# Performance work log

Measured on AMD Instinct MI355X. Metric: run time of the kernel, lower is better.

Reference implementation:

```python
import jax, jax.numpy as jnp
import numpy as np
import math

EMBED = 1024
HEADS = 16
DHEAD = 64
B, S = 2, 2048


def setup_inputs() -> dict:
    key = jax.random.key(0)
    k1, k2, k3, k4 = jax.random.split(key, 4)
    qs = jax.random.normal(k1, (B, S, EMBED), dtype=jnp.float32)
    # causal mask, broadcast over batch (mask==0 positions are masked out)
    mask = jnp.broadcast_to(jnp.tril(jnp.ones((S, S), dtype=jnp.int32)), (B, S, S))
    # torch Linear(embed, 3*H*D, bias=False): y = x @ W^T; store transposed [E, 3HD]
    Wqkv = jax.random.normal(k2, (EMBED, 3 * HEADS * DHEAD), dtype=jnp.float32) / math.sqrt(EMBED)
    Wout = jax.random.normal(k3, (HEADS * DHEAD, EMBED), dtype=jnp.float32) / math.sqrt(HEADS * DHEAD)
    bout = jax.random.normal(k4, (EMBED,), dtype=jnp.float32) * 0.01
    return {"qs": qs, "mask": mask, "Wqkv": Wqkv, "Wout": Wout, "bout": bout}


def reference(qs, mask, Wqkv, Wout, bout):
    b, s, _ = qs.shape
    # fused QKV projection -> (B, S, 3H, D), split into q/k/v chunks of H heads
    qkv = (qs @ Wqkv).reshape(b, s, 3 * HEADS, DHEAD)
    q, k, v = qkv[:, :, :HEADS], qkv[:, :, HEADS:2 * HEADS], qkv[:, :, 2 * HEADS:]
    # scores: (B, H, Sq, Sk)
    scores = jnp.einsum("bqhd,bkhd->bhqk", q, k) / math.sqrt(DHEAD)
    scores = jnp.where(mask[:, None, :, :] == 0, jnp.float32(-1e9), scores)
    attn = jax.nn.softmax(scores, axis=-1)
    out = jnp.einsum("bhqk,bkhd->bqhd", attn, v).reshape(b, s, HEADS * DHEAD)
    return out @ Wout + bout
```

## Files before the change

kernel.cpp:

```cpp
#include <hip/hip_runtime.h>
#include <hip/hip_bf16.h>
#include <stdint.h>


typedef __attribute__((ext_vector_type(8))) short  short8;
typedef __attribute__((ext_vector_type(4))) short  short4v;
typedef __attribute__((ext_vector_type(4))) float  float4v;

#define SOFTMAX_BIAS 17.3123405f
#define QSCALE 0.18033688f

__device__ __forceinline__ unsigned short f2bf(float f) {
  unsigned int u = __builtin_bit_cast(unsigned int, f);
  u += 0x7fffu + ((u >> 16) & 1u);
  return (unsigned short)(u >> 16);
}
__device__ __forceinline__ unsigned short f2bf_trunc(float f) {
  return (unsigned short)(__builtin_bit_cast(unsigned int, f) >> 16);
}
__device__ __forceinline__ float bf2f(unsigned short s) {
  unsigned int u = ((unsigned int)s) << 16;
  return __builtin_bit_cast(float, u);
}

__device__ __forceinline__ void async_copy16(const void* g, void* l) {
  __builtin_amdgcn_global_load_lds(
      (__attribute__((address_space(1))) unsigned int*)g,
      (__attribute__((address_space(3))) unsigned int*)l, 16, 0, 0);
}

__global__ void prep_kernel(const float* __restrict__ qs,
                            const float* __restrict__ Wqkv,
                            const float* __restrict__ Wout,
                            unsigned short* __restrict__ qs_bf,
                            unsigned short* __restrict__ WqkvT,
                            unsigned short* __restrict__ WoutT) {
  __shared__ float tbuf[32][33];
  const int blk = blockIdx.x, tid = threadIdx.x;
  if (blk < 4096) {
    int i = (blk * 256 + tid) * 4;
    float4v v = *(const float4v*)(qs + i);
    short4v o;
    o[0] = (short)f2bf(v[0]); o[1] = (short)f2bf(v[1]);
    o[2] = (short)f2bf(v[2]); o[3] = (short)f2bf(v[3]);
    *(short4v*)(qs_bf + i) = o;
  } else {
    const float* W; unsigned short* Wt; int N, t;
    if (blk < 4096 + 3072) { W = Wqkv; Wt = WqkvT; N = 3072; t = blk - 4096; }
    else                   { W = Wout; Wt = WoutT; N = 1024; t = blk - 7168; }
    const int tilesx = N >> 5;
    const int n0 = (t % tilesx) * 32, k0 = (t / tilesx) * 32;
    const int x = tid & 31, y = tid >> 5;
#pragma unroll
    for (int i = 0; i < 4; ++i)
      tbuf[y + i * 8][x] = W[(size_t)(k0 + y + i * 8) * N + n0 + x];
    __syncthreads();
#pragma unroll
    for (int i = 0; i < 4; ++i)
      Wt[(size_t)(n0 + y + i * 8) * 1024 + k0 + x] = f2bf(tbuf[x][y + i * 8]);
  }
}

__device__ __forceinline__ void gemm_bt_core(const unsigned short* __restrict__ A,
                                             const unsigned short* __restrict__ Bt,
                                             int m0, int n0,
                                             short* As, short* Bs,
                                             float4v (&acc)[4][4],
                                             int wm, int wn, int l15, int quad,
                                             int tid) {
  for (int k0 = 0; k0 < 1024; k0 += 32) {
    __syncthreads();
#pragma unroll
    for (int i = 0; i < 2; ++i) {
      int u = i * 256 + tid;
      int r = u >> 2, cpw = u & 3;
      int c = cpw ^ ((r >> 1) & 3);
      async_copy16(A  + (size_t)(m0 + r) * 1024 + k0 + c * 8, As + u * 8);
      async_copy16(Bt + (size_t)(n0 + r) * 1024 + k0 + c * 8, Bs + u * 8);
    }
    __syncthreads();

    short8 af[4], bfv[4];
#pragma unroll
    for (int t = 0; t < 4; ++t) {
      int ra = wm * 64 + t * 16 + l15;
      af[t]  = *(const short8*)(As + (ra * 4 + (quad ^ ((ra >> 1) & 3))) * 8);
      int rb = wn * 64 + t * 16 + l15;
      bfv[t] = *(const short8*)(Bs + (rb * 4 + (quad ^ ((rb >> 1) & 3))) * 8);
    }
#pragma unroll
    for (int mt = 0; mt < 4; ++mt)
#pragma unroll
      for (int nt = 0; nt < 4; ++nt)
        acc[mt][nt] = __builtin_amdgcn_mfma_f32_16x16x32_bf16(
            af[mt], bfv[nt], acc[mt][nt], 0, 0, 0);
  }
}

__global__ __launch_bounds__(256, 3)
void gemm_qkv_kernel(const unsigned short* __restrict__ Aq,
                     const unsigned short* __restrict__ Bt,
                     unsigned short* __restrict__ Qb,
                     unsigned short* __restrict__ Kb,
                     unsigned short* __restrict__ Vb) {
  __shared__ short As[128 * 32];
  __shared__ short Bs[128 * 32];
  const int tid = threadIdx.x, lane = tid & 63, w = tid >> 6;
  const int wm = w & 1, wn = w >> 1, l15 = lane & 15, quad = lane >> 4;
  const int m0 = blockIdx.x * 128, n0 = blockIdx.y * 128;

  float4v acc[4][4];
#pragma unroll
  for (int i = 0; i < 4; ++i)
#pragma unroll
    for (int j = 0; j < 4; ++j) acc[i][j] = (float4v)0.0f;

  gemm_bt_core(Aq, Bt, m0, n0, As, Bs, acc, wm, wn, l15, quad, tid);

#pragma unroll
  for (int nt = 0; nt < 4; ++nt) {
    int gn = n0 + wn * 64 + nt * 16 + l15;
    int j = gn >> 6, d = gn & 63;
    int g = j >> 4, h = j & 15;
    if (g == 2) {
#pragma unroll
      for (int mt = 0; mt < 4; ++mt) {
        int s0 = m0 + wm * 64 + mt * 16 + quad * 4;
        int b = s0 >> 11, s = s0 & 2047;
        short4v pk;
        pk[0] = (short)f2bf(acc[mt][nt][0]);
        pk[1] = (short)f2bf(acc[mt][nt][1]);
        pk[2] = (short)f2bf(acc[mt][nt][2]);
        pk[3] = (short)f2bf(acc[mt][nt][3]);
        *(short4v*)(Vb + (((size_t)(b * 16 + h) * 64 + d) << 11) + s) = pk;
      }
    } else {
#pragma unroll
      for (int mt = 0; mt < 4; ++mt) {
#pragma unroll
        for (int r = 0; r < 4; ++r) {
          int gm = m0 + wm * 64 + mt * 16 + quad * 4 + r;
          int b = gm >> 11, s = gm & 2047;
          float v = acc[mt][nt][r];
          if (g == 0)
            Qb[(((size_t)(b * 16 + h) * 2048 + s) << 6) + d] = f2bf(v * QSCALE);
          else
            Kb[(((size_t)(b * 16 + h) * 2048 + s) << 6) + d] = f2bf(v);
        }
      }
    }
  }
}

__global__ __launch_bounds__(256, 2)
void flash_attn_kernel(const unsigned short* __restrict__ Qb,
                       const unsigned short* __restrict__ Kb,
                       const unsigned short* __restrict__ Vb,
                       unsigned short* __restrict__ Pp0,
                       unsigned short* __restrict__ Pp1,
                       float* __restrict__ lws) {
  __shared__ unsigned short Kt[128 * 64];
  __shared__ unsigned short Vt[64 * 128];

  const int tid = threadIdx.x, lane = tid & 63, w = tid >> 6;
  const int l15 = lane & 15, quad = lane >> 4;
  const int rank = blockIdx.x >> 6;
  const int qt = 15 - rank;
  const int rem = blockIdx.x & 63;
  const int half = rem & 1;
  const int bh = rem >> 1;
  const int bb = bh >> 4, h = bh & 15;

  const int n = qt + 1, nh0 = (n + 1) >> 1;
  const int kt_lo = half ? nh0 : 0;
  const int kt_hi = half ? n : nh0;

  const unsigned short* Qg = Qb + (size_t)bh * 2048 * 64;
  const unsigned short* Kg = Kb + (size_t)bh * 2048 * 64;
  const unsigned short* Vg = Vb + (size_t)bh * 64 * 2048;
  unsigned short* Pw = Kt + w * (32 * 64);

  const int qb0 = qt * 128 + w * 32;

  short8 qf[2][2];
#pragma unroll
  for (int nt = 0; nt < 2; ++nt)
#pragma unroll
    for (int kc = 0; kc < 2; ++kc)
      qf[nt][kc] = *(const short8*)(Qg + (size_t)(qb0 + nt * 16 + l15) * 64 +
                                    kc * 32 + quad * 8);

  float l_s[2] = {0.0f, 0.0f};
  float4v o[4][2];
#pragma unroll
  for (int i = 0; i < 4; ++i) { o[i][0] = (float4v)0.0f; o[i][1] = (float4v)0.0f; }

  short8 kstg[4];
  if (kt_lo < kt_hi) {
#pragma unroll
    for (int j = 0; j < 4; ++j) {
      int u = j * 256 + tid;
      int r = u >> 3, cp = u & 7;
      kstg[j] = *(const short8*)(Kg + (size_t)(kt_lo * 128 + r) * 64 +
                                 (cp ^ (r & 7)) * 8);
    }
  }

  for (int kt = kt_lo; kt < kt_hi; ++kt) {
    const int kb = kt * 128;
    __syncthreads();
#pragma unroll
    for (int j = 0; j < 4; ++j)
      *(short8*)(Kt + (j * 256 + tid) * 8) = kstg[j];
    __syncthreads();
#pragma unroll
    for (int i = 0; i < 4; ++i) {
      int u = i * 256 + tid;
      int r2 = u >> 4, cp2 = u & 15;
      async_copy16(Vg + (size_t)r2 * 2048 + kb + (cp2 ^ (r2 & 15)) * 8, Vt + u * 8);
    }
    {
      int ktn = (kt + 1 < kt_hi) ? kt + 1 : kt;
#pragma unroll
      for (int j = 0; j < 4; ++j) {
        int u = j * 256 + tid;
        int r = u >> 3, cp = u & 7;
        kstg[j] = *(const short8*)(Kg + (size_t)(ktn * 128 + r) * 64 +
                                   (cp ^ (r & 7)) * 8);
      }
    }

    float4v st[8][2];
    __builtin_amdgcn_s_setprio(1);
#pragma unroll
    for (int mt = 0; mt < 8; ++mt) {
      st[mt][0] = (float4v)(-SOFTMAX_BIAS);
      st[mt][1] = (float4v)(-SOFTMAX_BIAS);
      int key = mt * 16 + l15;
#pragma unroll
      for (int kc = 0; kc < 2; ++kc) {
        int cp = (kc * 4 + quad) ^ (key & 7);
        short8 a = *(const short8*)(Kt + key * 64 + cp * 8);
        st[mt][0] = __builtin_amdgcn_mfma_f32_16x16x32_bf16(a, qf[0][kc], st[mt][0], 0, 0, 0);
        st[mt][1] = __builtin_amdgcn_mfma_f32_16x16x32_bf16(a, qf[1][kc], st[mt][1], 0, 0, 0);
      }
    }
    __builtin_amdgcn_s_setprio(0);

    if (kt == qt) {
#pragma unroll
      for (int nt = 0; nt < 2; ++nt) {
        int qg = qb0 + nt * 16 + l15;
#pragma unroll
        for (int mt = 0; mt < 8; ++mt)
#pragma unroll
          for (int r = 0; r < 4; ++r) {
            int keyg = kb + mt * 16 + quad * 4 + r;
            if (keyg > qg) st[mt][nt][r] = -1e5f;
          }
      }
    }

#pragma unroll
    for (int nt = 0; nt < 2; ++nt) {
      float sum = 0.0f;
#pragma unroll
      for (int mt = 0; mt < 8; ++mt)
#pragma unroll
        for (int r = 0; r < 4; ++r) {
          float p = __builtin_amdgcn_exp2f(st[mt][nt][r]);
          st[mt][nt][r] = p;
          sum += p;
        }
      l_s[nt] += sum;
    }

    __syncthreads();

#pragma unroll
    for (int hf = 0; hf < 2; ++hf) {
#pragma unroll
      for (int nt = 0; nt < 2; ++nt) {
        int ql = nt * 16 + l15;
        unsigned short* prow = Pw + ql * 64;
#pragma unroll
        for (int mtl = 0; mtl < 4; ++mtl) {
          int mt = hf * 4 + mtl;
          short4v pk;
          pk[0] = (short)f2bf_trunc(st[mt][nt][0]);
          pk[1] = (short)f2bf_trunc(st[mt][nt][1]);
          pk[2] = (short)f2bf_trunc(st[mt][nt][2]);
          pk[3] = (short)f2bf_trunc(st[mt][nt][3]);
          int cp = (mtl * 2 + (quad >> 1)) ^ (l15 & 7);
          *(short4v*)(prow + cp * 8 + (quad & 1) * 4) = pk;
        }
      }
      __builtin_amdgcn_s_setprio(1);
#pragma unroll
      for (int kcl = 0; kcl < 2; ++kcl) {
        int kcg = hf * 2 + kcl;
        short8 pb[2];
#pragma unroll
        for (int nt = 0; nt < 2; ++nt) {
          int ql = nt * 16 + l15;
          int cp = (kcl * 4 + quad) ^ (l15 & 7);
          pb[nt] = *(const short8*)(Pw + ql * 64 + cp * 8);
        }
#pragma unroll
        for (int mtd = 0; mtd < 4; ++mtd) {
          int d = mtd * 16 + l15;
          int cp2 = (kcg * 4 + quad) ^ (d & 15);
          short8 a = *(const short8*)(Vt + d * 128 + cp2 * 8);
          o[mtd][0] = __builtin_amdgcn_mfma_f32_16x16x32_bf16(a, pb[0], o[mtd][0], 0, 0, 0);
          o[mtd][1] = __builtin_amdgcn_mfma_f32_16x16x32_bf16(a, pb[1], o[mtd][1], 0, 0, 0);
        }
      }
      __builtin_amdgcn_s_setprio(0);
    }
  }

  unsigned short* Pp = half ? Pp1 : Pp0;
#pragma unroll
  for (int nt = 0; nt < 2; ++nt) {
    float l = l_s[nt];
    l += __shfl_xor(l, 16);
    l += __shfl_xor(l, 32);
    int qg = qb0 + nt * 16 + l15;
    if (quad == 0) lws[half * 65536 + bh * 2048 + qg] = l;
#pragma unroll
    for (int mtd = 0; mtd < 4; ++mtd) {
      short4v pk;
      pk[0] = (short)f2bf(o[mtd][nt][0]);
      pk[1] = (short)f2bf(o[mtd][nt][1]);
      pk[2] = (short)f2bf(o[mtd][nt][2]);
      pk[3] = (short)f2bf(o[mtd][nt][3]);
      *(short4v*)(Pp + (size_t)(bb * 2048 + qg) * 1024 + h * 64 + mtd * 16 +
                  quad * 4) = pk;
    }
  }
}

__global__ void combine_kernel(const unsigned short* __restrict__ P0,
                               unsigned short* __restrict__ P1,
                               const float* __restrict__ lws) {
  int idx = (blockIdx.x * 256 + threadIdx.x) * 8;
  int t = idx >> 10, c = idx & 1023;
  int bh = (t >> 11) * 16 + (c >> 6);
  int q = t & 2047;
  float inv = 1.0f / (lws[bh * 2048 + q] + lws[65536 + bh * 2048 + q]);
  short8 a = *(const short8*)(P0 + idx);
  short8 b = *(const short8*)(P1 + idx);
  short8 r;
#pragma unroll
  for (int j = 0; j < 8; ++j)
    r[j] = (short)f2bf((bf2f((unsigned short)a[j]) +
                        bf2f((unsigned short)b[j])) * inv);
  *(short8*)(P1 + idx) = r;
}

__global__ __launch_bounds__(256, 3)
void gemm_out_kernel(const unsigned short* __restrict__ Aq,
                     const unsigned short* __restrict__ Bt,
                     const float* __restrict__ bout,
                     float* __restrict__ out) {
  __shared__ short As[64 * 32];
  __shared__ short Bs[128 * 32];
  const int tid = threadIdx.x, lane = tid & 63, w = tid >> 6;
  const int wm = w & 1, wn = w >> 1, l15 = lane & 15, quad = lane >> 4;
  const int m0 = blockIdx.x * 64, n0 = blockIdx.y * 128;

  float4v acc[2][4];
#pragma unroll
  for (int i = 0; i < 2; ++i)
#pragma unroll
    for (int j = 0; j < 4; ++j) acc[i][j] = (float4v)0.0f;

  for (int k0 = 0; k0 < 1024; k0 += 32) {
    __syncthreads();
    {
      int u = tid;
      int r = u >> 2, cpw = u & 3;
      int c = cpw ^ ((r >> 1) & 3);
      async_copy16(Aq + (size_t)(m0 + r) * 1024 + k0 + c * 8, As + u * 8);
    }
#pragma unroll
    for (int i = 0; i < 2; ++i) {
      int u = i * 256 + tid;
      int r = u >> 2, cpw = u & 3;
      int c = cpw ^ ((r >> 1) & 3);
      async_copy16(Bt + (size_t)(n0 + r) * 1024 + k0 + c * 8, Bs + u * 8);
    }
    __syncthreads();

    short8 af[2], bfv[4];
#pragma unroll
    for (int t = 0; t < 2; ++t) {
      int ra = wm * 32 + t * 16 + l15;
      af[t] = *(const short8*)(As + (ra * 4 + (quad ^ ((ra >> 1) & 3))) * 8);
    }
#pragma unroll
    for (int t = 0; t < 4; ++t) {
      int rbx = wn * 64 + t * 16 + l15;
      bfv[t] = *(const short8*)(Bs + (rbx * 4 + (quad ^ ((rbx >> 1) & 3))) * 8);
    }
#pragma unroll
    for (int mt = 0; mt < 2; ++mt)
#pragma unroll
      for (int nt = 0; nt < 4; ++nt)
        acc[mt][nt] = __builtin_amdgcn_mfma_f32_16x16x32_bf16(
            af[mt], bfv[nt], acc[mt][nt], 0, 0, 0);
  }

#pragma unroll
  for (int nt = 0; nt < 4; ++nt) {
    int gn = n0 + wn * 64 + nt * 16 + l15;
    float bias = bout[gn];
#pragma unroll
    for (int mt = 0; mt < 2; ++mt) {
      int gmb = m0 + wm * 32 + mt * 16 + quad * 4;
#pragma unroll
      for (int r = 0; r < 4; ++r)
        out[(size_t)(gmb + r) * 1024 + gn] = acc[mt][nt][r] + bias;
    }
  }
}

extern "C" void kernel_launch(void* const* d_in, const int* in_sizes, int n_in,
                              void* d_out, int out_size, void* d_ws, size_t ws_size,
                              hipStream_t stream) {
  (void)in_sizes; (void)n_in; (void)out_size; (void)ws_size;
  const float* qs   = (const float*)d_in[0];
  const float* Wqkv = (const float*)d_in[2];
  const float* Wout = (const float*)d_in[3];
  const float* bout = (const float*)d_in[4];
  float* out = (float*)d_out;

  unsigned short* qs_bf = (unsigned short*)d_ws;
  unsigned short* WqkvT = qs_bf + 4096 * 1024;
  unsigned short* WoutT = WqkvT + 3072 * 1024;
  unsigned short* Qb    = WoutT + 1024 * 1024;
  unsigned short* Kb    = Qb + 32 * 2048 * 64;
  unsigned short* Vb    = Kb + 32 * 2048 * 64;
  unsigned short* Ob    = Vb + 32 * 2048 * 64;

  unsigned short* P0 = qs_bf;
  float*          lw = (float*)WqkvT;
  unsigned short* P1 = Ob;

  prep_kernel<<<8192, 256, 0, stream>>>(qs, Wqkv, Wout, qs_bf, WqkvT, WoutT);
  gemm_qkv_kernel<<<dim3(32, 24), 256, 0, stream>>>(qs_bf, WqkvT, Qb, Kb, Vb);
  flash_attn_kernel<<<1024, 256, 0, stream>>>(Qb, Kb, Vb, P0, P1, lw);
  combine_kernel<<<2048, 256, 0, stream>>>(P0, P1, lw);
  gemm_out_kernel<<<dim3(64, 8), 256, 0, stream>>>(P1, WoutT, bout, out);
}
```

Baseline: 188.6 us.

## Fuse split-KV combine into flash attention via last-arriver atomic flag

Removes the separate combine kernel. Each flash-attention block that finishes its half of a split-KV tile bumps an atomic counter per (batch-head, q-tile). The second block to arrive reads the partner's partial output and row sum, normalizes, and writes the final bf16 result. The flags are zeroed in prep_kernel. This saves a kernel launch and one full read/write pass over the two partial buffers, in exchange for fences, an atomic, and some extra epilogue work in the attention kernel.

```diff
diff --git a/kernel.cpp b/kernel.cpp
--- a/kernel.cpp
+++ b/kernel.cpp
@@ -34,7 +34,8 @@
                             const float* __restrict__ Wout,
                             unsigned short* __restrict__ qs_bf,
                             unsigned short* __restrict__ WqkvT,
-                            unsigned short* __restrict__ WoutT) {
+                            unsigned short* __restrict__ WoutT,
+                            int* __restrict__ flags) {
   __shared__ float tbuf[32][33];
   const int blk = blockIdx.x, tid = threadIdx.x;
   if (blk < 4096) {
@@ -45,6 +46,10 @@
     o[2] = (short)f2bf(v[2]); o[3] = (short)f2bf(v[3]);
     *(short4v*)(qs_bf + i) = o;
   } else {
+    if (blk == 4096) {
+      flags[tid] = 0;
+      flags[tid + 256] = 0;
+    }
     const float* W; unsigned short* Wt; int N, t;
     if (blk < 4096 + 3072) { W = Wqkv; Wt = WqkvT; N = 3072; t = blk - 4096; }
     else                   { W = Wout; Wt = WoutT; N = 1024; t = blk - 7168; }
@@ -158,7 +163,8 @@
                        const unsigned short* __restrict__ Vb,
                        unsigned short* __restrict__ Pp0,
                        unsigned short* __restrict__ Pp1,
-                       float* __restrict__ lws) {
+                       float* __restrict__ lws,
+                       int* __restrict__ flags) {
   __shared__ unsigned short Kt[128 * 64];
   __shared__ unsigned short Vt[64 * 128];
 
@@ -320,11 +326,13 @@
   }
 
   unsigned short* Pp = half ? Pp1 : Pp0;
+  float l_tot[2];
 #pragma unroll
   for (int nt = 0; nt < 2; ++nt) {
     float l = l_s[nt];
     l += __shfl_xor(l, 16);
     l += __shfl_xor(l, 32);
+    l_tot[nt] = l;
     int qg = qb0 + nt * 16 + l15;
     if (quad == 0) lws[half * 65536 + bh * 2048 + qg] = l;
 #pragma unroll
@@ -338,24 +346,30 @@
                   quad * 4) = pk;
     }
   }
-}
-
-__global__ void combine_kernel(const unsigned short* __restrict__ P0,
-                               unsigned short* __restrict__ P1,
-                               const float* __restrict__ lws) {
-  int idx = (blockIdx.x * 256 + threadIdx.x) * 8;
-  int t = idx >> 10, c = idx & 1023;
-  int bh = (t >> 11) * 16 + (c >> 6);
-  int q = t & 2047;
-  float inv = 1.0f / (lws[bh * 2048 + q] + lws[65536 + bh * 2048 + q]);
-  short8 a = *(const short8*)(P0 + idx);
-  short8 b = *(const short8*)(P1 + idx);
-  short8 r;
-#pragma unroll
-  for (int j = 0; j < 8; ++j)
-    r[j] = (short)f2bf((bf2f((unsigned short)a[j]) +
-                        bf2f((unsigned short)b[j])) * inv);
-  *(short8*)(P1 + idx) = r;
+
+  __threadfence();
+  __shared__ int who_s;
+  if (tid == 0) who_s = atomicAdd(&flags[(bh << 4) + qt], 1);
+  __syncthreads();
+  if (who_s == 0) return;
+  __threadfence();
+  const unsigned short* Po = half ? Pp0 : Pp1;
+  const float* lo = lws + (half ? 0 : 65536) + bh * 2048;
+#pragma unroll
+  for (int nt = 0; nt < 2; ++nt) {
+    int qg = qb0 + nt * 16 + l15;
+    float inv = 1.0f / (l_tot[nt] + lo[qg]);
+#pragma unroll
+    for (int mtd = 0; mtd < 4; ++mtd) {
+      size_t off = (size_t)(bb * 2048 + qg) * 1024 + h * 64 + mtd * 16 + quad * 4;
+      short4v ov = *(const short4v*)(Po + off);
+      short4v pk;
+#pragma unroll
+      for (int r = 0; r < 4; ++r)
+        pk[r] = (short)f2bf((o[mtd][nt][r] + bf2f((unsigned short)ov[r])) * inv);
+      *(short4v*)(Pp1 + off) = pk;
+    }
+  }
 }
 
 __global__ __launch_bounds__(256, 3)
@@ -442,14 +456,14 @@
   unsigned short* Kb    = Qb + 32 * 2048 * 64;
   unsigned short* Vb    = Kb + 32 * 2048 * 64;
   unsigned short* Ob    = Vb + 32 * 2048 * 64;
+  int*            flg   = (int*)(Ob + 4096 * 1024);
 
   unsigned short* P0 = qs_bf;
   float*          lw = (float*)WqkvT;
   unsigned short* P1 = Ob;
 
-  prep_kernel<<<8192, 256, 0, stream>>>(qs, Wqkv, Wout, qs_bf, WqkvT, WoutT);
+  prep_kernel<<<8192, 256, 0, stream>>>(qs, Wqkv, Wout, qs_bf, WqkvT, WoutT, flg);
   gemm_qkv_kernel<<<dim3(32, 24), 256, 0, stream>>>(qs_bf, WqkvT, Qb, Kb, Vb);
-  flash_attn_kernel<<<1024, 256, 0, stream>>>(Qb, Kb, Vb, P0, P1, lw);
-  combine_kernel<<<2048, 256, 0, stream>>>(P0, P1, lw);
+  flash_attn_kernel<<<1024, 256, 0, stream>>>(Qb, Kb, Vb, P0, P1, lw, flg);
   gemm_out_kernel<<<dim3(64, 8), 256, 0, stream>>>(P1, WoutT, bout, out);
 }
```

Result: slower. 436.3 us (+131.3%).
